# Kernel optimization log

Hardware: AMD Instinct MI355X
Metric: run time of the kernel (lower is better)

## Reference

```python
import jax, jax.numpy as jnp
import numpy as np

N = 50000   # nodes per graph
E = 800000  # edges per graph
FIN = 128   # node_features
H = 4       # heads
C = 32      # out channels per head (hidden_dim // heads)
HID = H * C # 128
FE = 16     # edge_features
B = 8       # graphs in batch
NEG_SLOPE = 0.2


def setup_inputs() -> dict:
    key = jax.random.key(0)
    ks = jax.random.split(key, 30)
    f32 = jnp.float32
    inp = {
        'x_a': jax.random.normal(ks[0], (N, FIN), f32),
        'edge_index_a': jax.random.randint(ks[1], (2, E), 0, N),
        'edge_attr_a': jax.random.normal(ks[2], (E, FE), f32),
        'batch_a': jnp.sort(jax.random.randint(ks[3], (N,), 0, B)),
        'x_b': jax.random.normal(ks[4], (N, FIN), f32),
        'edge_index_b': jax.random.randint(ks[5], (2, E), 0, N),
        'edge_attr_b': jax.random.normal(ks[6], (E, FE), f32),
        'batch_b': jnp.sort(jax.random.randint(ks[7], (N,), 0, B)),
    }
    def p(i, shape, s=0.05):
        return jax.random.normal(ks[i], shape, f32) * s
    # GAT layer 1 (in FIN -> H*C)
    inp['W1l'] = p(8, (FIN, HID)); inp['b1l'] = jnp.zeros((HID,), f32)
    inp['W1r'] = p(9, (FIN, HID)); inp['b1r'] = jnp.zeros((HID,), f32)
    inp['W1e'] = p(10, (FE, HID))
    inp['att1'] = p(11, (H, C))
    inp['bias1'] = jnp.zeros((HID,), f32)
    # GAT layer 2 (in HID -> H*C)
    inp['W2l'] = p(12, (HID, HID)); inp['b2l'] = jnp.zeros((HID,), f32)
    inp['W2r'] = p(13, (HID, HID)); inp['b2r'] = jnp.zeros((HID,), f32)
    inp['W2e'] = p(14, (FE, HID))
    inp['att2'] = p(15, (H, C))
    inp['bias2'] = jnp.zeros((HID,), f32)
    # fc head: Linear(4*HID, HID) -> ReLU -> Linear(HID, 1)
    inp['Wf1'] = p(16, (4 * HID, HID)); inp['bf1'] = jnp.zeros((HID,), f32)
    inp['Wf2'] = p(17, (HID, 1)); inp['bf2'] = jnp.zeros((1,), f32)
    return inp


def gatv2(x, edge_index, edge_attr, Wl, bl, Wr, br, We, att, bias):
    """GATv2Conv (concat=True), eval mode (no dropout)."""
    src, dst = edge_index[0], edge_index[1]
    n = x.shape[0]
    xl = (x @ Wl + bl).reshape(n, H, C)  # source transform
    xr = (x @ Wr + br).reshape(n, H, C)  # target transform
    # per-edge pre-activation: x_j + x_i + edge_emb  -> [E, H, C]
    m = xl[src] + xr[dst] + (edge_attr @ We).reshape(-1, H, C)
    logits = jnp.einsum('ehc,hc->eh', jax.nn.leaky_relu(m, NEG_SLOPE), att)  # [E, H]
    # scatter-softmax over incoming edges of each destination node
    lmax = jax.ops.segment_max(logits, dst, num_segments=n)
    lmax = jnp.where(jnp.isfinite(lmax), lmax, 0.0)
    ex = jnp.exp(logits - lmax[dst])
    denom = jax.ops.segment_sum(ex, dst, num_segments=n)
    alpha = ex / (denom[dst] + 1e-16)  # [E, H]
    out = jax.ops.segment_sum(alpha[:, :, None] * xl[src], dst, num_segments=n)  # [N, H, C]
    return out.reshape(n, HID) + bias


def encode(x, edge_index, edge_attr, batch,
           W1l, b1l, W1r, b1r, W1e, att1, bias1,
           W2l, b2l, W2r, b2r, W2e, att2, bias2):
    h = jax.nn.elu(gatv2(x, edge_index, edge_attr, W1l, b1l, W1r, b1r, W1e, att1, bias1))
    h = jax.nn.elu(gatv2(h, edge_index, edge_attr, W2l, b2l, W2r, b2r, W2e, att2, bias2))
    cnt = jnp.clip(jax.ops.segment_sum(jnp.ones((h.shape[0],), h.dtype), batch, num_segments=B), 1.0)
    h_mean = jax.ops.segment_sum(h, batch, num_segments=B) / cnt[:, None]
    h_max = jax.ops.segment_max(h, batch, num_segments=B)
    h_max = jnp.where(jnp.isfinite(h_max), h_max, 0.0)
    return jnp.concatenate([h_mean, h_max], axis=-1)  # [B, 2*HID]


def reference(x_a, edge_index_a, edge_attr_a, batch_a,
              x_b, edge_index_b, edge_attr_b, batch_b,
              W1l, b1l, W1r, b1r, W1e, att1, bias1,
              W2l, b2l, W2r, b2r, W2e, att2, bias2,
              Wf1, bf1, Wf2, bf2):
    emb_a = encode(x_a, edge_index_a, edge_attr_a, batch_a,
                   W1l, b1l, W1r, b1r, W1e, att1, bias1,
                   W2l, b2l, W2r, b2r, W2e, att2, bias2)
    emb_b = encode(x_b, edge_index_b, edge_attr_b, batch_b,
                   W1l, b1l, W1r, b1r, W1e, att1, bias1,
                   W2l, b2l, W2r, b2r, W2e, att2, bias2)
    combined = jnp.concatenate([emb_a, emb_b], axis=-1)  # [B, 4*HID]
    hidden = jax.nn.relu(combined @ Wf1 + bf1)
    dominance = jax.nn.sigmoid(hidden @ Wf2 + bf2).squeeze(-1)  # [B]
    return dominance
```

## Files before the change

kernel.cpp:

```cpp
#include <hip/hip_runtime.h>
#include <hip/hip_fp16.h>

#define NN 50000
#define NE 800000
#define HIDD 128
#define FEAT_E 16
#define NGRAPH 8
#define CAP 64
#define GATBLK 1280

typedef __attribute__((ext_vector_type(2))) _Float16 half2_t;
typedef __attribute__((ext_vector_type(8))) _Float16 half8_t;
typedef __attribute__((ext_vector_type(4))) float floatx4;


__device__ __forceinline__ unsigned int fenc(float f) {
  unsigned int u = __float_as_uint(f);
  return (u & 0x80000000u) ? ~u : (u | 0x80000000u);
}
__device__ __forceinline__ float fdec(unsigned int u) {
  if (u == 0u) return 0.0f;
  float f = (u & 0x80000000u) ? __uint_as_float(u & 0x7fffffffu)
                              : __uint_as_float(~u);
  return __builtin_isfinite(f) ? f : 0.0f;
}

__device__ __forceinline__ half8_t splat8(_Float16 v) {
  return (half8_t){v, v, v, v, v, v, v, v};
}
__device__ __forceinline__ half8_t hmax8(half8_t a, half8_t b) {
#if __has_builtin(__builtin_elementwise_max)
  return __builtin_elementwise_max(a, b);
#else
  half8_t r;
#pragma unroll
  for (int i = 0; i < 8; ++i) r[i] = a[i] > b[i] ? a[i] : b[i];
  return r;
#endif
}
__device__ __forceinline__ float dot_att(half8_t lk, half2_t t01, half2_t t23,
                                         half2_t t45, half2_t t67) {
#if __has_builtin(__builtin_amdgcn_fdot2)
  float p = __builtin_amdgcn_fdot2((half2_t){lk[0], lk[1]}, t01, 0.f, false);
  p = __builtin_amdgcn_fdot2((half2_t){lk[2], lk[3]}, t23, p, false);
  p = __builtin_amdgcn_fdot2((half2_t){lk[4], lk[5]}, t45, p, false);
  p = __builtin_amdgcn_fdot2((half2_t){lk[6], lk[7]}, t67, p, false);
  return p;
#else
  float p = 0.f;
  p += (float)lk[0] * (float)t01[0] + (float)lk[1] * (float)t01[1];
  p += (float)lk[2] * (float)t23[0] + (float)lk[3] * (float)t23[1];
  p += (float)lk[4] * (float)t45[0] + (float)lk[5] * (float)t45[1];
  p += (float)lk[6] * (float)t67[0] + (float)lk[7] * (float)t67[1];
  return p;
#endif
}

__global__ void prep_wt_k(const float* __restrict__ Wl, const float* __restrict__ Wr,
                          _Float16* __restrict__ wtg) {
  const int r = blockIdx.x & 127;
  const int which = blockIdx.x >> 7;
  const int k = threadIdx.x;
  const float* W = which ? Wr : Wl;
  const int oc_src = (r & 15) * 8 + (r >> 4);
  const int col = k ^ ((r & 7) << 3);
  wtg[(which * 128 + r) * 128 + col] = (_Float16)W[k * 128 + oc_src];
}

__device__ __forceinline__ half8_t load_a8(const _Float16* p) {
  return *(const half8_t*)p;
}
__device__ __forceinline__ half8_t load_a8(const float* p) {
  const float4 f0 = *(const float4*)p;
  const float4 f1 = *(const float4*)(p + 4);
  return (half8_t){(_Float16)f0.x, (_Float16)f0.y, (_Float16)f0.z, (_Float16)f0.w,
                   (_Float16)f1.x, (_Float16)f1.y, (_Float16)f1.z, (_Float16)f1.w};
}

template <typename TIN>
__global__ __launch_bounds__(256) void node_linear_mfma_k(
    const TIN* __restrict__ x, const _Float16* __restrict__ wtg,
    const float* __restrict__ bl, const float* __restrict__ br,
    _Float16* __restrict__ xl16, _Float16* __restrict__ xr16) {
  __shared__ _Float16 wt[128 * 128];
  const int tid = threadIdx.x;
  const int which = blockIdx.y;
  const _Float16* wsrc = wtg + which * (128 * 128);
  const float* bias128 = which ? br : bl;
  _Float16* out = which ? xr16 : xl16;
  {
    const half8_t* src = (const half8_t*)wsrc;
    half8_t* dstl = (half8_t*)wt;
#pragma unroll
    for (int it = 0; it < 8; ++it)
      dstl[it * 256 + tid] = src[it * 256 + tid];
  }
  __syncthreads();

  const int wv = tid >> 6, lane = tid & 63;
  const int arow = lane & 15, kq = lane >> 4;
  const int nbase = blockIdx.x * 64 + wv * 16;
  int nload = nbase + arow;
  if (nload >= NN) nload = NN - 1;
  floatx4 acc[8];
#pragma unroll
  for (int t = 0; t < 8; ++t) acc[t] = (floatx4){0.f, 0.f, 0.f, 0.f};
#pragma unroll
  for (int kb = 0; kb < 4; ++kb) {
    const half8_t a = load_a8(x + (size_t)nload * 128 + kb * 32 + kq * 8);
    const int colbase = (kb * 32 + kq * 8) ^ ((arow & 7) << 3);
#pragma unroll
    for (int t = 0; t < 8; ++t) {
      const half8_t b = *(const half8_t*)&wt[(t * 16 + arow) * 128 + colbase];
      acc[t] = __builtin_amdgcn_mfma_f32_16x16x32_f16(a, b, acc[t], 0, 0, 0);
    }
  }
  const float4 bv0 = *(const float4*)&bias128[arow * 8];
  const float4 bv1 = *(const float4*)&bias128[arow * 8 + 4];
  const float bv[8] = {bv0.x, bv0.y, bv0.z, bv0.w, bv1.x, bv1.y, bv1.z, bv1.w};
#pragma unroll
  for (int i = 0; i < 4; ++i) {
    const int n = nbase + kq * 4 + i;
    if (n < NN) {
      half8_t v;
#pragma unroll
      for (int t = 0; t < 8; ++t) v[t] = (_Float16)(acc[t][i] + bv[t]);
      *(half8_t*)(out + (size_t)n * 128 + arow * 8) = v;
    }
  }
}

__global__ void build_k(const int* __restrict__ src, const int* __restrict__ dst,
                        const float* __restrict__ eattr,
                        int* __restrict__ cnt, int2* __restrict__ bpair,
                        _Float16* __restrict__ eatt16) {
  const int e = blockIdx.x * blockDim.x + threadIdx.x;
  if (e >= NE) return;
  const float4* ea = (const float4*)(eattr + (size_t)e * FEAT_E);
  const float4 a0 = ea[0], a1 = ea[1], a2 = ea[2], a3 = ea[3];
  half8_t h0 = {(_Float16)a0.x, (_Float16)a0.y, (_Float16)a0.z, (_Float16)a0.w,
                (_Float16)a1.x, (_Float16)a1.y, (_Float16)a1.z, (_Float16)a1.w};
  half8_t h1 = {(_Float16)a2.x, (_Float16)a2.y, (_Float16)a2.z, (_Float16)a2.w,
                (_Float16)a3.x, (_Float16)a3.y, (_Float16)a3.z, (_Float16)a3.w};
  half8_t* eo = (half8_t*)(eatt16 + (size_t)e * FEAT_E);
  eo[0] = h0; eo[1] = h1;
  const int d = dst[e];
  const int pos = atomicAdd(&cnt[d], 1);
  if (pos < CAP) bpair[(size_t)d * CAP + pos] = make_int2(src[e], e);
}

__global__ __launch_bounds__(256) void node_gat_fused_k(
    const _Float16* __restrict__ xl16, const _Float16* __restrict__ xr16,
    const _Float16* __restrict__ eatt16,
    const int2* __restrict__ bpair, const int* __restrict__ cnt,
    const float* __restrict__ We, const float* __restrict__ att,
    const float* __restrict__ bias, _Float16* __restrict__ hout) {
  __shared__ half8_t WeS[FEAT_E][16];
  const int tid = threadIdx.x;
  {
    const int f = tid >> 4, q = tid & 15;
    const float4 w0 = ((const float4*)We)[f * 32 + q * 2];
    const float4 w1 = ((const float4*)We)[f * 32 + q * 2 + 1];
    WeS[f][q] = (half8_t){(_Float16)w0.x, (_Float16)w0.y, (_Float16)w0.z, (_Float16)w0.w,
                          (_Float16)w1.x, (_Float16)w1.y, (_Float16)w1.z, (_Float16)w1.w};
  }
  __syncthreads();

  const int wave = tid >> 6, lane = tid & 63;
  const int slot = lane >> 4, l16 = lane & 15;
  constexpr int NW = GATBLK * 4;

  const float4 af0 = ((const float4*)att)[l16 * 2];
  const float4 af1 = ((const float4*)att)[l16 * 2 + 1];
  const half2_t at01 = {(_Float16)af0.x, (_Float16)af0.y};
  const half2_t at23 = {(_Float16)af0.z, (_Float16)af0.w};
  const half2_t at45 = {(_Float16)af1.x, (_Float16)af1.y};
  const half2_t at67 = {(_Float16)af1.z, (_Float16)af1.w};
  const float4 bi0 = ((const float4*)bias)[l16 * 2];
  const float4 bi1 = ((const float4*)bias)[l16 * 2 + 1];

  int d = blockIdx.x * 4 + wave;
  int degA = cnt[d];
  degA = degA < CAP ? degA : CAP;
  int dB = d + NW;
  int degB_raw = 0;
  if (dB < NN) degB_raw = cnt[dB];
  int2 mypA = make_int2(0, 0);
  if (lane < degA) mypA = bpair[(size_t)d * CAP + lane];
  half8_t xrhA = *(const half8_t*)(xr16 + (size_t)d * HIDD + l16 * 8);

#define FINISH_EDGE(XL, EM, VALID)                                       \
  {                                                                      \
    half8_t m_ = ((XL) + xrh) + (EM);                                    \
    half8_t lk_ = hmax8(m_, m_ * splat8((_Float16)0.2f));                \
    float p_ = dot_att(lk_, at01, at23, at45, at67);                     \
    p_ += __shfl_xor(p_, 1);                                             \
    p_ += __shfl_xor(p_, 2);                                             \
    const float w_ = (VALID) ? __expf(p_) : 0.f;                         \
    den += w_;                                                           \
    acc0 = fmaf(w_, (float)(XL)[0], acc0);                               \
    acc1 = fmaf(w_, (float)(XL)[1], acc1);                               \
    acc2 = fmaf(w_, (float)(XL)[2], acc2);                               \
    acc3 = fmaf(w_, (float)(XL)[3], acc3);                               \
    acc4 = fmaf(w_, (float)(XL)[4], acc4);                               \
    acc5 = fmaf(w_, (float)(XL)[5], acc5);                               \
    acc6 = fmaf(w_, (float)(XL)[6], acc6);                               \
    acc7 = fmaf(w_, (float)(XL)[7], acc7);                               \
  }

#define LOAD_PAIR_AT(E0, E1, X0, X1, A0, B0, A1, B1)                     \
  {                                                                      \
    const int s0_ = __shfl(myp.x, (E0)), i0_ = __shfl(myp.y, (E0));      \
    const int s1_ = __shfl(myp.x, (E1)), i1_ = __shfl(myp.y, (E1));      \
    X0 = *(const half8_t*)(xl16 + (unsigned)s0_ * 128u + l16 * 8);       \
    X1 = *(const half8_t*)(xl16 + (unsigned)s1_ * 128u + l16 * 8);       \
    A0 = *(const half8_t*)(eatt16 + (unsigned)i0_ * 16u);                \
    B0 = *(const half8_t*)(eatt16 + (unsigned)i0_ * 16u + 8u);           \
    A1 = *(const half8_t*)(eatt16 + (unsigned)i1_ * 16u);                \
    B1 = *(const half8_t*)(eatt16 + (unsigned)i1_ * 16u + 8u);           \
  }

#define COMPUTE_PAIR()                                                   \
  {                                                                      \
    half8_t em0 = {}, em1 = {};                                          \
    _Pragma("unroll") for (int f = 0; f < 8; ++f) {                      \
      const half8_t wf = WeS[f][l16];                                    \
      em0 += splat8(a0[f]) * wf;                                         \
      em1 += splat8(a1[f]) * wf;                                         \
    }                                                                    \
    _Pragma("unroll") for (int f = 0; f < 8; ++f) {                      \
      const half8_t wf = WeS[8 + f][l16];                                \
      em0 += splat8(b0[f]) * wf;                                         \
      em1 += splat8(b1[f]) * wf;                                         \
    }                                                                    \
    FINISH_EDGE(x0, em0, e0 < deg)                                       \
    FINISH_EDGE(x1, em1, e1 < deg)                                       \
  }

  for (;;) {
    const int deg = degA;
    const int2 myp = mypA;
    const half8_t xrh = xrhA;
    float acc0 = 0.f, acc1 = 0.f, acc2 = 0.f, acc3 = 0.f;
    float acc4 = 0.f, acc5 = 0.f, acc6 = 0.f, acc7 = 0.f;
    float den = 0.f;

    const int T = (deg + 7) >> 3;
    int e0 = slot, e1 = slot + 4;
    half8_t x0, x1, a0, b0, a1, b1;
    if (T > 0) {
      LOAD_PAIR_AT(e0, e1, x0, x1, a0, b0, a1, b1)
    }
    const int dC = dB + NW;
    int degB = degB_raw < CAP ? degB_raw : CAP;
    int degC_raw = 0;
    int2 mypB = make_int2(0, 0);
    half8_t xrhB = {};
    if (dB < NN) {
      if (dC < NN) degC_raw = cnt[dC];
      if (lane < degB) mypB = bpair[(size_t)dB * CAP + lane];
      xrhB = *(const half8_t*)(xr16 + (size_t)dB * HIDD + l16 * 8);
    }
    if (T > 0) {
      for (int k = 0; k + 1 < T; ++k) {
        half8_t nx0, nx1, na0, nb0, na1, nb1;
        LOAD_PAIR_AT(e0 + 8, e1 + 8, nx0, nx1, na0, nb0, na1, nb1)
        COMPUTE_PAIR()
        e0 += 8; e1 += 8;
        x0 = nx0; x1 = nx1; a0 = na0; b0 = nb0; a1 = na1; b1 = nb1;
      }
      const bool pairLast = (((T - 1) << 3) + 4) < deg;
      if (pairLast) {
        COMPUTE_PAIR()
      } else {
        half8_t em0 = {};
#pragma unroll
        for (int f = 0; f < 8; ++f) em0 += splat8(a0[f]) * WeS[f][l16];
#pragma unroll
        for (int f = 0; f < 8; ++f) em0 += splat8(b0[f]) * WeS[8 + f][l16];
        FINISH_EDGE(x0, em0, e0 < deg)
      }
    }

#define RED(A) A += __shfl_xor(A, 16); A += __shfl_xor(A, 32);
    RED(acc0) RED(acc1) RED(acc2) RED(acc3)
    RED(acc4) RED(acc5) RED(acc6) RED(acc7)
    RED(den)
#undef RED
    if (slot == 0) {
      const float inv = 1.f / (den + 1e-16f);
      float o0 = fmaf(acc0, inv, bi0.x), o1 = fmaf(acc1, inv, bi0.y);
      float o2 = fmaf(acc2, inv, bi0.z), o3 = fmaf(acc3, inv, bi0.w);
      float o4 = fmaf(acc4, inv, bi1.x), o5 = fmaf(acc5, inv, bi1.y);
      float o6 = fmaf(acc6, inv, bi1.z), o7 = fmaf(acc7, inv, bi1.w);
      o0 = o0 > 0.f ? o0 : expm1f(o0);  o1 = o1 > 0.f ? o1 : expm1f(o1);
      o2 = o2 > 0.f ? o2 : expm1f(o2);  o3 = o3 > 0.f ? o3 : expm1f(o3);
      o4 = o4 > 0.f ? o4 : expm1f(o4);  o5 = o5 > 0.f ? o5 : expm1f(o5);
      o6 = o6 > 0.f ? o6 : expm1f(o6);  o7 = o7 > 0.f ? o7 : expm1f(o7);
      half8_t ho = {(_Float16)o0, (_Float16)o1, (_Float16)o2, (_Float16)o3,
                    (_Float16)o4, (_Float16)o5, (_Float16)o6, (_Float16)o7};
      *(half8_t*)(hout + (size_t)d * HIDD + l16 * 8) = ho;
    }

    if (dB >= NN) break;
    d = dB; degA = degB; mypA = mypB; xrhA = xrhB;
    dB = dC; degB_raw = degC_raw;
  }
#undef COMPUTE_PAIR
#undef LOAD_PAIR_AT
#undef FINISH_EDGE
}

__global__ void pool_k(const _Float16* __restrict__ h, const int* __restrict__ batch,
                       float* __restrict__ gsum, unsigned int* __restrict__ gmax,
                       float* __restrict__ gcnt) {
  __shared__ float ssum[NGRAPH][HIDD];
  __shared__ float smax[NGRAPH][HIDD];
  __shared__ float scnt[NGRAPH];
  const int t = threadIdx.x;
#pragma unroll
  for (int g = 0; g < NGRAPH; ++g) {
    ssum[g][t] = 0.f;
    smax[g][t] = -3.0e38f;
  }
  if (t < NGRAPH) scnt[t] = 0.f;
  __syncthreads();
  const int n0 = blockIdx.x * 64;
  const int nEnd = (n0 + 64 < NN) ? (n0 + 64) : NN;
  unsigned int seen = 0;
  for (int n = n0; n < nEnd; ++n) {
    const int g = batch[n];
    seen |= 1u << g;
    const float v = (float)h[(size_t)n * HIDD + t];
    ssum[g][t] += v;
    smax[g][t] = fmaxf(smax[g][t], v);
    if (t == 0) scnt[g] += 1.f;
  }
  __syncthreads();
  for (int g = 0; g < NGRAPH; ++g) {
    if (seen & (1u << g)) {
      atomicAdd(&gsum[g * HIDD + t], ssum[g][t]);
      atomicMax(&gmax[g * HIDD + t], fenc(smax[g][t]));
      if (t == 0) atomicAdd(&gcnt[g], scnt[g]);
    }
  }
}

__global__ void head_k(const float* __restrict__ suma, const unsigned int* __restrict__ maxa,
                       const float* __restrict__ cnta,
                       const float* __restrict__ sumb, const unsigned int* __restrict__ maxb,
                       const float* __restrict__ cntb,
                       const float* __restrict__ Wf1, const float* __restrict__ bf1,
                       const float* __restrict__ Wf2, const float* __restrict__ bf2,
                       float* __restrict__ out) {
  __shared__ float c[4 * HIDD];
  __shared__ float red[HIDD];
  const int g = blockIdx.x, t = threadIdx.x;
  const float ca = fmaxf(cnta[g], 1.f), cb = fmaxf(cntb[g], 1.f);
  c[t]            = suma[g * HIDD + t] / ca;
  c[HIDD + t]     = fdec(maxa[g * HIDD + t]);
  c[2 * HIDD + t] = sumb[g * HIDD + t] / cb;
  c[3 * HIDD + t] = fdec(maxb[g * HIDD + t]);
  __syncthreads();
  float acc = bf1[t];
  for (int i = 0; i < 4 * HIDD; ++i)
    acc = fmaf(c[i], Wf1[(size_t)i * HIDD + t], acc);
  acc = fmaxf(acc, 0.f);
  red[t] = acc * Wf2[t];
  __syncthreads();
  for (int s2 = 64; s2 > 0; s2 >>= 1) {
    if (t < s2) red[t] += red[t + s2];
    __syncthreads();
  }
  if (t == 0) out[g] = 1.f / (1.f + expf(-(red[0] + bf2[0])));
}

extern "C" void kernel_launch(void* const* d_in, const int* in_sizes, int n_in,
                              void* d_out, int out_size, void* d_ws, size_t ws_size,
                              hipStream_t stream) {
  (void)in_sizes; (void)n_in; (void)out_size; (void)ws_size;
  const float* xA    = (const float*)d_in[0];
  const int*   eiA   = (const int*)  d_in[1];
  const float* eaA   = (const float*)d_in[2];
  const int*   batA  = (const int*)  d_in[3];
  const float* xB    = (const float*)d_in[4];
  const int*   eiB   = (const int*)  d_in[5];
  const float* eaB   = (const float*)d_in[6];
  const int*   batB  = (const int*)  d_in[7];
  const float* W1l   = (const float*)d_in[8];
  const float* b1l   = (const float*)d_in[9];
  const float* W1r   = (const float*)d_in[10];
  const float* b1r   = (const float*)d_in[11];
  const float* W1e   = (const float*)d_in[12];
  const float* att1  = (const float*)d_in[13];
  const float* bias1 = (const float*)d_in[14];
  const float* W2l   = (const float*)d_in[15];
  const float* b2l   = (const float*)d_in[16];
  const float* W2r   = (const float*)d_in[17];
  const float* b2r   = (const float*)d_in[18];
  const float* W2e   = (const float*)d_in[19];
  const float* att2  = (const float*)d_in[20];
  const float* bias2 = (const float*)d_in[21];
  const float* Wf1   = (const float*)d_in[22];
  const float* bf1   = (const float*)d_in[23];
  const float* Wf2   = (const float*)d_in[24];
  const float* bf2   = (const float*)d_in[25];

  char* ws = (char*)d_ws;
  size_t off = 0;
  auto alloc = [&](size_t bytes) -> void* {
    void* p = ws + off;
    off += (bytes + 255) & ~(size_t)255;
    return p;
  };
  _Float16* h16    = (_Float16*)alloc((size_t)NN * HIDD * 2);
  _Float16* xl16   = (_Float16*)alloc((size_t)NN * HIDD * 2);
  _Float16* xr16   = (_Float16*)alloc((size_t)NN * HIDD * 2);
  int2*     bpair  = (int2*)    alloc((size_t)NN * CAP * 8);
  _Float16* eatt16 = (_Float16*)alloc((size_t)NE * FEAT_E * 2);
  int*      cnt    = (int*)     alloc((size_t)NN * 4);
  _Float16* wtg1   = (_Float16*)alloc(2 * 128 * 128 * 2);
  _Float16* wtg2   = (_Float16*)alloc(2 * 128 * 128 * 2);
  const size_t poolStart = off;
  float*        psumA = (float*)alloc(NGRAPH * HIDD * 4);
  unsigned int* pmaxA = (unsigned int*)alloc(NGRAPH * HIDD * 4);
  float*        pcntA = (float*)alloc(NGRAPH * 4);
  float*        psumB = (float*)alloc(NGRAPH * HIDD * 4);
  unsigned int* pmaxB = (unsigned int*)alloc(NGRAPH * HIDD * 4);
  float*        pcntB = (float*)alloc(NGRAPH * 4);
  const size_t poolBytes = off - poolStart;

  const float* xs[2]   = {xA, xB};
  const int*   eis[2]  = {eiA, eiB};
  const float* eas[2]  = {eaA, eaB};
  const int*   bats[2] = {batA, batB};
  float*        psums[2] = {psumA, psumB};
  unsigned int* pmaxs[2] = {pmaxA, pmaxB};
  float*        pcnts[2] = {pcntA, pcntB};

  hipMemsetAsync(psumA, 0, poolBytes, stream);
  prep_wt_k<<<256, 128, 0, stream>>>(W1l, W1r, wtg1);
  prep_wt_k<<<256, 128, 0, stream>>>(W2l, W2r, wtg2);

  for (int g = 0; g < 2; ++g) {
    const int* src = eis[g];
    const int* dst = eis[g] + NE;
    hipMemsetAsync(cnt, 0, (size_t)NN * 4, stream);
    build_k<<<NE / 256, 256, 0, stream>>>(src, dst, eas[g], cnt, bpair, eatt16);
    node_linear_mfma_k<float><<<dim3((NN + 63) / 64, 2), 256, 0, stream>>>(
        xs[g], wtg1, b1l, b1r, xl16, xr16);
    node_gat_fused_k<<<GATBLK, 256, 0, stream>>>(xl16, xr16, eatt16, bpair, cnt,
                                                 W1e, att1, bias1, h16);
    node_linear_mfma_k<_Float16><<<dim3((NN + 63) / 64, 2), 256, 0, stream>>>(
        h16, wtg2, b2l, b2r, xl16, xr16);
    node_gat_fused_k<<<GATBLK, 256, 0, stream>>>(xl16, xr16, eatt16, bpair, cnt,
                                                 W2e, att2, bias2, h16);
    pool_k<<<(NN + 63) / 64, 128, 0, stream>>>(h16, bats[g], psums[g], pmaxs[g], pcnts[g]);
  }
  head_k<<<NGRAPH, 128, 0, stream>>>(psumA, pmaxA, pcntA, psumB, pmaxB, pcntB,
                                     Wf1, bf1, Wf2, bf2, (float*)d_out);
}
```

Before: 800.0 us.

## Replace static node striding in GAT kernel with atomic work-queue partitions

The fused GAT node kernel now hands out destination nodes dynamically: each wave takes its next node index from one of 8 partitioned atomic counters, with a three-deep lookahead, instead of a fixed grid stride. Because node degrees vary, the aim is better load balance across waves and less tail imbalance. In exchange it adds an atomic per node per wave and a counter buffer that must be zeroed for every launch, and it may reduce memory locality because node order becomes dynamic.

```diff
diff --git a/kernel.cpp b/kernel.cpp
--- a/kernel.cpp
+++ b/kernel.cpp
@@ -8,6 +8,9 @@
 #define NGRAPH 8
 #define CAP 64
 #define GATBLK 1280
+#define NQPART 8
+#define NPART (NN / NQPART)
+#define QSTRIDE 32
 
 typedef __attribute__((ext_vector_type(2))) _Float16 half2_t;
 typedef __attribute__((ext_vector_type(8))) _Float16 half8_t;
@@ -154,7 +157,8 @@
     const _Float16* __restrict__ eatt16,
     const int2* __restrict__ bpair, const int* __restrict__ cnt,
     const float* __restrict__ We, const float* __restrict__ att,
-    const float* __restrict__ bias, _Float16* __restrict__ hout) {
+    const float* __restrict__ bias, _Float16* __restrict__ hout,
+    int* __restrict__ qctr) {
   __shared__ half8_t WeS[FEAT_E][16];
   const int tid = threadIdx.x;
   {
@@ -166,9 +170,11 @@
   }
   __syncthreads();
 
-  const int wave = tid >> 6, lane = tid & 63;
+  const int lane = tid & 63;
   const int slot = lane >> 4, l16 = lane & 15;
-  constexpr int NW = GATBLK * 4;
+  const int part = blockIdx.x & (NQPART - 1);
+  const int nbase = part * NPART;
+  int* ctr = qctr + part * QSTRIDE;
 
   const float4 af0 = ((const float4*)att)[l16 * 2];
   const float4 af1 = ((const float4*)att)[l16 * 2 + 1];
@@ -179,15 +185,24 @@
   const float4 bi0 = ((const float4*)bias)[l16 * 2];
   const float4 bi1 = ((const float4*)bias)[l16 * 2 + 1];
 
-  int d = blockIdx.x * 4 + wave;
-  int degA = cnt[d];
-  degA = degA < CAP ? degA : CAP;
-  int dB = d + NW;
-  int degB_raw = 0;
-  if (dB < NN) degB_raw = cnt[dB];
+  int pA = 0, pB = 0, pC = 0;
+  if (lane == 0) {
+    pA = atomicAdd(ctr, 1);
+    pB = atomicAdd(ctr, 1);
+    pC = atomicAdd(ctr, 1);
+  }
+  pA = __shfl(pA, 0); pB = __shfl(pB, 0); pC = __shfl(pC, 0);
+
+  int dA = nbase + (pA < NPART ? pA : 0);
+  int degA = 0;
+  if (pA < NPART) {
+    degA = cnt[dA];
+    degA = degA < CAP ? degA : CAP;
+  }
+  int degB_raw = (pB < NPART) ? cnt[nbase + pB] : 0;
   int2 mypA = make_int2(0, 0);
-  if (lane < degA) mypA = bpair[(size_t)d * CAP + lane];
-  half8_t xrhA = *(const half8_t*)(xr16 + (size_t)d * HIDD + l16 * 8);
+  if (lane < degA) mypA = bpair[(size_t)dA * CAP + lane];
+  half8_t xrhA = *(const half8_t*)(xr16 + (size_t)dA * HIDD + l16 * 8);
 
 #define FINISH_EDGE(XL, EM, VALID)                                       \
   {                                                                      \
@@ -237,7 +252,7 @@
     FINISH_EDGE(x1, em1, e1 < deg)                                       \
   }
 
-  for (;;) {
+  while (pA < NPART) {
     const int deg = degA;
     const int2 myp = mypA;
     const half8_t xrh = xrhA;
@@ -251,16 +266,18 @@
     if (T > 0) {
       LOAD_PAIR_AT(e0, e1, x0, x1, a0, b0, a1, b1)
     }
-    const int dC = dB + NW;
+    const int degC_raw = cnt[nbase + (pC < NPART ? pC : 0)];
+    int pD = 0;
+    if (lane == 0) pD = atomicAdd(ctr, 1);
+    pD = __shfl(pD, 0);
+    const bool bOK = (pB < NPART);
+    const int dB = nbase + (bOK ? pB : 0);
     int degB = degB_raw < CAP ? degB_raw : CAP;
-    int degC_raw = 0;
+    if (!bOK) degB = 0;
     int2 mypB = make_int2(0, 0);
-    half8_t xrhB = {};
-    if (dB < NN) {
-      if (dC < NN) degC_raw = cnt[dC];
-      if (lane < degB) mypB = bpair[(size_t)dB * CAP + lane];
-      xrhB = *(const half8_t*)(xr16 + (size_t)dB * HIDD + l16 * 8);
-    }
+    if (lane < degB) mypB = bpair[(size_t)dB * CAP + lane];
+    half8_t xrhB = *(const half8_t*)(xr16 + (size_t)dB * HIDD + l16 * 8);
+
     if (T > 0) {
       for (int k = 0; k + 1 < T; ++k) {
         half8_t nx0, nx1, na0, nb0, na1, nb1;
@@ -299,12 +316,12 @@
       o6 = o6 > 0.f ? o6 : expm1f(o6);  o7 = o7 > 0.f ? o7 : expm1f(o7);
       half8_t ho = {(_Float16)o0, (_Float16)o1, (_Float16)o2, (_Float16)o3,
                     (_Float16)o4, (_Float16)o5, (_Float16)o6, (_Float16)o7};
-      *(half8_t*)(hout + (size_t)d * HIDD + l16 * 8) = ho;
-    }
-
-    if (dB >= NN) break;
-    d = dB; degA = degB; mypA = mypB; xrhA = xrhB;
-    dB = dC; degB_raw = degC_raw;
+      *(half8_t*)(hout + (size_t)dA * HIDD + l16 * 8) = ho;
+    }
+
+    pA = pB; dA = dB; degA = degB; mypA = mypB; xrhA = xrhB;
+    pB = pC; degB_raw = degC_raw;
+    pC = pD;
   }
 #undef COMPUTE_PAIR
 #undef LOAD_PAIR_AT
@@ -421,6 +438,7 @@
   int*      cnt    = (int*)     alloc((size_t)NN * 4);
   _Float16* wtg1   = (_Float16*)alloc(2 * 128 * 128 * 2);
   _Float16* wtg2   = (_Float16*)alloc(2 * 128 * 128 * 2);
+  int*      qctr   = (int*)     alloc(4 * NQPART * QSTRIDE * 4);
   const size_t poolStart = off;
   float*        psumA = (float*)alloc(NGRAPH * HIDD * 4);
   unsigned int* pmaxA = (unsigned int*)alloc(NGRAPH * HIDD * 4);
@@ -439,9 +457,11 @@
   float*        pcnts[2] = {pcntA, pcntB};
 
   hipMemsetAsync(psumA, 0, poolBytes, stream);
+  hipMemsetAsync(qctr, 0, 4 * NQPART * QSTRIDE * 4, stream);
   prep_wt_k<<<256, 128, 0, stream>>>(W1l, W1r, wtg1);
   prep_wt_k<<<256, 128, 0, stream>>>(W2l, W2r, wtg2);
 
+  int launchIdx = 0;
   for (int g = 0; g < 2; ++g) {
     const int* src = eis[g];
     const int* dst = eis[g] + NE;
@@ -449,12 +469,14 @@
     build_k<<<NE / 256, 256, 0, stream>>>(src, dst, eas[g], cnt, bpair, eatt16);
     node_linear_mfma_k<float><<<dim3((NN + 63) / 64, 2), 256, 0, stream>>>(
         xs[g], wtg1, b1l, b1r, xl16, xr16);
-    node_gat_fused_k<<<GATBLK, 256, 0, stream>>>(xl16, xr16, eatt16, bpair, cnt,
-                                                 W1e, att1, bias1, h16);
+    node_gat_fused_k<<<GATBLK, 256, 0, stream>>>(
+        xl16, xr16, eatt16, bpair, cnt, W1e, att1, bias1, h16,
+        qctr + (launchIdx++) * NQPART * QSTRIDE);
     node_linear_mfma_k<_Float16><<<dim3((NN + 63) / 64, 2), 256, 0, stream>>>(
         h16, wtg2, b2l, b2r, xl16, xr16);
-    node_gat_fused_k<<<GATBLK, 256, 0, stream>>>(xl16, xr16, eatt16, bpair, cnt,
-                                                 W2e, att2, bias2, h16);
+    node_gat_fused_k<<<GATBLK, 256, 0, stream>>>(
+        xl16, xr16, eatt16, bpair, cnt, W2e, att2, bias2, h16,
+        qctr + (launchIdx++) * NQPART * QSTRIDE);
     pool_k<<<(NN + 63) / 64, 128, 0, stream>>>(h16, bats[g], psums[g], pmaxs[g], pcnts[g]);
   }
   head_k<<<NGRAPH, 128, 0, stream>>>(psumA, pmaxA, pcntA, psumB, pmaxB, pcntB,
```

Measured after the change: 966.0 us. 20.8% more time.
